# Kernel tuning notes

Hardware: AMD Instinct MI355X
Metric: run time of the kernel (lower is better)

Reference implementation:

```python
import jax, jax.numpy as jnp
import numpy as np

NUM_HEADS = 16


def setup_inputs() -> dict:
    key = jax.random.key(0)
    ks = jax.random.split(key, 7)
    B, N, D = 16, 512, 1024
    return {
        "x": jax.random.normal(ks[0], (B, N, D), dtype=jnp.float32),
        "spatial_encoding": jax.random.normal(ks[1], (B, N, N), dtype=jnp.float32),
        "edge_encoding": jax.random.normal(ks[2], (B, N, N), dtype=jnp.float32),
        "Wq": jax.random.normal(ks[3], (D, D), dtype=jnp.float32) * (D ** -0.5),
        "Wk": jax.random.normal(ks[4], (D, D), dtype=jnp.float32) * (D ** -0.5),
        "Wv": jax.random.normal(ks[5], (D, D), dtype=jnp.float32) * (D ** -0.5),
        "Wo": jax.random.normal(ks[6], (D, D), dtype=jnp.float32) * (D ** -0.5),
    }


def reference(x, spatial_encoding, edge_encoding, Wq, Wk, Wv, Wo):
    B, N, D = x.shape
    H = NUM_HEADS
    hd = D // H
    scale = D ** -0.5  # NOTE: source scales by hidden_dim**-0.5, not head_size**-0.5

    def split_heads(t):  # (B,N,D) -> (B,H,N,hd)
        return t.reshape(B, N, H, hd).transpose(0, 2, 1, 3)

    q = split_heads(x @ Wq.T)
    k = split_heads(x @ Wk.T)
    v = split_heads(x @ Wv.T)

    bias = (spatial_encoding + edge_encoding)[:, None]  # (B,1,N,N)
    a = jnp.einsum("bhnd,bhmd->bhnm", q, k) * scale + bias  # (B,H,N,N)

    # rows that are entirely zero (padded) are masked to -inf
    row_nonzero = jnp.any(a != 0, axis=-1, keepdims=True)  # (B,H,N,1)
    a = jnp.where(row_nonzero, a, -jnp.inf)
    p = jax.nn.softmax(a, axis=-1)
    p = jnp.where(jnp.isnan(p), 0.0, p)  # nan_to_num after softmax of all -inf rows

    o = jnp.einsum("bhnm,bhmd->bhnd", p, v)  # (B,H,N,hd)
    o = o.transpose(0, 2, 1, 3).reshape(B, N, D)
    return o @ Wo.T
```

## Files before the change

### kernel.cpp

```cpp
#include <hip/hip_runtime.h>
#include <cstdint>


typedef unsigned short u16;
typedef unsigned int   u32;
typedef __attribute__((ext_vector_type(8))) short bf8;
typedef __attribute__((ext_vector_type(4))) float f4;

__device__ __forceinline__ u16 f2bf(float x) {
  u32 u = __float_as_uint(x);
  u += 0x7FFF + ((u >> 16) & 1);
  return (u16)(u >> 16);
}

__device__ __forceinline__ float bf2f(u16 x) {
  return __uint_as_float(((u32)x) << 16);
}

__device__ __forceinline__ void gl2lds16(const void* g, void* l) {
  __builtin_amdgcn_global_load_lds(
      (const __attribute__((address_space(1))) u32*)g,
      (__attribute__((address_space(3))) u32*)l, 16, 0, 0);
}


__global__ __launch_bounds__(256) void cast_bf16(const float* __restrict__ src,
                                                 uint4* __restrict__ dst, int n8) {
  const int i = blockIdx.x * 256 + threadIdx.x;
  if (i >= n8) return;
  const float4* s = (const float4*)src;
  const float4 a = s[2 * i], c = s[2 * i + 1];
  uint4 o;
  o.x = (u32)f2bf(a.x) | ((u32)f2bf(a.y) << 16);
  o.y = (u32)f2bf(a.z) | ((u32)f2bf(a.w) << 16);
  o.z = (u32)f2bf(c.x) | ((u32)f2bf(c.y) << 16);
  o.w = (u32)f2bf(c.z) | ((u32)f2bf(c.w) << 16);
  dst[i] = o;
}

__global__ __launch_bounds__(256) void cast4_bf16(
    const float* __restrict__ s0, const float* __restrict__ s1,
    const float* __restrict__ s2, const float* __restrict__ s3,
    uint4* __restrict__ d0, uint4* __restrict__ d1,
    uint4* __restrict__ d2, uint4* __restrict__ d3) {
  const int i = blockIdx.x * 256 + threadIdx.x;
  const int w = i >> 17, j = i & 131071;
  const float* src = (w == 0) ? s0 : (w == 1) ? s1 : (w == 2) ? s2 : s3;
  uint4* dst = (w == 0) ? d0 : (w == 1) ? d1 : (w == 2) ? d2 : d3;
  const float4* s = (const float4*)src;
  const float4 a = s[2 * j], c = s[2 * j + 1];
  uint4 o;
  o.x = (u32)f2bf(a.x) | ((u32)f2bf(a.y) << 16);
  o.y = (u32)f2bf(a.z) | ((u32)f2bf(a.w) << 16);
  o.z = (u32)f2bf(c.x) | ((u32)f2bf(c.y) << 16);
  o.w = (u32)f2bf(c.z) | ((u32)f2bf(c.w) << 16);
  dst[j] = o;
}

__global__ __launch_bounds__(256) void bias_bf16(const float* __restrict__ s1,
                                                 const float* __restrict__ s2,
                                                 uint4* __restrict__ dst, int n8) {
  const int i = blockIdx.x * 256 + threadIdx.x;
  if (i >= n8) return;
  const float4* a4 = (const float4*)s1;
  const float4* b4 = (const float4*)s2;
  const float4 a = a4[2 * i], b = b4[2 * i];
  const float4 c = a4[2 * i + 1], d = b4[2 * i + 1];
  uint4 o;
  o.x = (u32)f2bf(a.x + b.x) | ((u32)f2bf(a.y + b.y) << 16);
  o.y = (u32)f2bf(a.z + b.z) | ((u32)f2bf(a.w + b.w) << 16);
  o.z = (u32)f2bf(c.x + d.x) | ((u32)f2bf(c.y + d.y) << 16);
  o.w = (u32)f2bf(c.z + d.z) | ((u32)f2bf(c.w + d.w) << 16);
  dst[i] = o;
}


__device__ __forceinline__ void gemm_core(const u16* __restrict__ A,
                                          const u16* __restrict__ Bt,
                                          int m0, int n0,
                                          u16* lA, u16* lB, f4 acc[4][4]) {
  const int tid  = threadIdx.x;
  const int wave = tid >> 6;
  const int lane = tid & 63;
  const int quad = lane >> 4;
  const int l16  = lane & 15;
  const int wm   = (wave >> 1) << 6;
  const int wn   = (wave & 1) << 6;
  const int srow = tid >> 3;
  const int scol = ((tid & 7) ^ (srow & 7)) << 3;
  const int c0   = (quad ^ (l16 & 7)) << 3;

  f4 zero = {0.f, 0.f, 0.f, 0.f};
#pragma unroll
  for (int mi = 0; mi < 4; mi++)
#pragma unroll
    for (int ni = 0; ni < 4; ni++) acc[mi][ni] = zero;

  const u16* Ab = A  + (size_t)(m0 + srow) * 1024 + scol;
  const u16* Bb = Bt + (size_t)(n0 + srow) * 1024 + scol;

  for (int k0 = 0; k0 < 1024; k0 += 64) {
    __syncthreads();
#pragma unroll
    for (int i = 0; i < 4; i++) {
      gl2lds16(Ab + (size_t)(i << 5) * 1024 + k0,
               (char*)lA + (((i << 8) + (wave << 6)) << 4));
      gl2lds16(Bb + (size_t)(i << 5) * 1024 + k0,
               (char*)lB + (((i << 8) + (wave << 6)) << 4));
    }
    __syncthreads();
#pragma unroll
    for (int kk = 0; kk < 64; kk += 32) {
      const int o = c0 ^ kk;
      bf8 af[4], bfr[4];
#pragma unroll
      for (int mi = 0; mi < 4; mi++)
        af[mi] = *(const bf8*)(lA + (wm + (mi << 4) + l16) * 64 + o);
#pragma unroll
      for (int ni = 0; ni < 4; ni++)
        bfr[ni] = *(const bf8*)(lB + (wn + (ni << 4) + l16) * 64 + o);
#pragma unroll
      for (int mi = 0; mi < 4; mi++)
#pragma unroll
        for (int ni = 0; ni < 4; ni++)
          acc[mi][ni] = __builtin_amdgcn_mfma_f32_16x16x32_bf16(
              af[mi], bfr[ni], acc[mi][ni], 0, 0, 0);
    }
  }
}


__global__ __launch_bounds__(256) void qkv_kernel(
    const u16* __restrict__ xb, const u16* __restrict__ wq,
    const u16* __restrict__ wk, const u16* __restrict__ wv,
    u16* __restrict__ Qh, u16* __restrict__ Kh, u16* __restrict__ Vt) {
  __shared__ __align__(16) u16 lA[128 * 64];
  __shared__ __align__(16) u16 lB[128 * 64];
  const int m0 = blockIdx.y << 7, n0 = blockIdx.x << 7;
  const int proj = blockIdx.z;
  const u16* W = (proj == 0) ? wq : (proj == 1) ? wk : wv;
  f4 acc[4][4];
  gemm_core(xb, W, m0, n0, lA, lB, acc);

  const int tid = threadIdx.x, wave = tid >> 6, lane = tid & 63;
  const int quad = lane >> 4, l16 = lane & 15;
  const int wm = (wave >> 1) << 6, wn = (wave & 1) << 6;

  if (proj == 2) {
#pragma unroll
    for (int mi = 0; mi < 4; mi++) {
      const int gmb = m0 + wm + (mi << 4) + (quad << 2);
      const int b = gmb >> 9, nb = gmb & 511;
#pragma unroll
      for (int ni = 0; ni < 4; ni++) {
        const int gn = n0 + wn + (ni << 4) + l16;
        const int h = gn >> 6, hdi = gn & 63;
        ushort4 pk;
        pk.x = f2bf(acc[mi][ni][0]);
        pk.y = f2bf(acc[mi][ni][1]);
        pk.z = f2bf(acc[mi][ni][2]);
        pk.w = f2bf(acc[mi][ni][3]);
        *(ushort4*)(Vt + ((size_t)((b << 4) + h) * 64 + hdi) * 512 + nb) = pk;
      }
    }
  } else {
    u16* dst = (proj == 0) ? Qh : Kh;
#pragma unroll
    for (int mi = 0; mi < 4; mi++) {
#pragma unroll
      for (int r = 0; r < 4; r++) {
        const int gm = m0 + wm + (mi << 4) + (quad << 2) + r;
        const int b = gm >> 9, n = gm & 511;
#pragma unroll
        for (int ni = 0; ni < 4; ni++) {
          const int gn = n0 + wn + (ni << 4) + l16;
          const int h = gn >> 6, hdi = gn & 63;
          dst[((size_t)((b << 4) + h) * 512 + n) * 64 + hdi] = f2bf(acc[mi][ni][r]);
        }
      }
    }
  }
}


__global__ __launch_bounds__(256) void oproj_kernel(const u16* __restrict__ Ob,
                                                    const u16* __restrict__ wo,
                                                    float* __restrict__ out) {
  __shared__ __align__(16) u16 lA[128 * 64];
  __shared__ __align__(16) u16 lB[128 * 64];
  const int m0 = blockIdx.y << 7, n0 = blockIdx.x << 7;
  f4 acc[4][4];
  gemm_core(Ob, wo, m0, n0, lA, lB, acc);

  const int tid = threadIdx.x, wave = tid >> 6, lane = tid & 63;
  const int quad = lane >> 4, l16 = lane & 15;
  const int wm = (wave >> 1) << 6, wn = (wave & 1) << 6;
#pragma unroll
  for (int mi = 0; mi < 4; mi++)
#pragma unroll
    for (int r = 0; r < 4; r++) {
      const int gm = m0 + wm + (mi << 4) + (quad << 2) + r;
#pragma unroll
      for (int ni = 0; ni < 4; ni++) {
        const int gn = n0 + wn + (ni << 4) + l16;
        out[(size_t)gm * 1024 + gn] = acc[mi][ni][r];
      }
    }
}


__global__ __launch_bounds__(256) void attn_kernel(
    const u16* __restrict__ Qh, const u16* __restrict__ Kh,
    const u16* __restrict__ Vt, const u16* __restrict__ Bb,
    u16* __restrict__ Ob) {
  __shared__ __align__(16) u16 sQ[64 * 64];
  __shared__ __align__(16) u16 sK[64 * 64];
  __shared__ __align__(16) u16 sV[64 * 64];
  __shared__ __align__(16) u16 sP[4 * 16 * 72];
  const int q0 = blockIdx.x << 6;
  const int h = blockIdx.y, b = blockIdx.z;
  const int tid = threadIdx.x, wave = tid >> 6, lane = tid & 63;
  const int quad = lane >> 4, l16 = lane & 15;
  const int c0  = (quad ^ (l16 & 7)) << 3;
  const int swb = (((tid & 7) ^ ((tid >> 3) & 7)) << 4);

  const u16* Qg = Qh + ((size_t)((b << 4) + h) * 512 + q0) * 64;
  const u16* Kg = Kh + (size_t)((b << 4) + h) * 512 * 64;
  const u16* Vg = Vt + (size_t)((b << 4) + h) * 64 * 512;
  const u16* Bg = Bb + (size_t)b * 512 * 512 + (size_t)q0 * 512;

#pragma unroll
  for (int i = 0; i < 2; i++) {
    const int e = (i << 8) + tid;
    gl2lds16((const char*)Qg + (e >> 3) * 128 + swb,
             (char*)sQ + (((i << 8) + (wave << 6)) << 4));
  }

  f4 o[4];
  f4 zero = {0.f, 0.f, 0.f, 0.f};
#pragma unroll
  for (int i = 0; i < 4; i++) o[i] = zero;
  float lsum[4] = {0.f, 0.f, 0.f, 0.f};
  const int qrl = (wave << 4) + (quad << 2);

  for (int j0 = 0; j0 < 512; j0 += 64) {
    __syncthreads();
#pragma unroll
    for (int i = 0; i < 2; i++) {
      const int e = (i << 8) + tid;
      gl2lds16((const char*)Kg + (size_t)j0 * 128 + (e >> 3) * 128 + swb,
               (char*)sK + (((i << 8) + (wave << 6)) << 4));
      gl2lds16((const char*)Vg + (size_t)(e >> 3) * 1024 + j0 * 2 + swb,
               (char*)sV + (((i << 8) + (wave << 6)) << 4));
    }
    __syncthreads();

    bf8 aq0 = *(const bf8*)(sQ + ((wave << 4) + l16) * 64 + c0);
    bf8 aq1 = *(const bf8*)(sQ + ((wave << 4) + l16) * 64 + (c0 ^ 32));
    u16* pw = sP + wave * (16 * 72);
#pragma unroll
    for (int nb = 0; nb < 4; nb++) {
      bf8 b0 = *(const bf8*)(sK + ((nb << 4) + l16) * 64 + c0);
      bf8 b1 = *(const bf8*)(sK + ((nb << 4) + l16) * 64 + (c0 ^ 32));
      f4 s = zero;
      s = __builtin_amdgcn_mfma_f32_16x16x32_bf16(aq0, b0, s, 0, 0, 0);
      s = __builtin_amdgcn_mfma_f32_16x16x32_bf16(aq1, b1, s, 0, 0, 0);
      const int gc = j0 + (nb << 4) + l16;
#pragma unroll
      for (int r = 0; r < 4; r++) {
        const float ev = __expf(s[r] * 0.03125f +
                                bf2f(Bg[(size_t)(qrl + r) * 512 + gc]));
        lsum[r] += ev;
        pw[((quad << 2) + r) * 72 + (nb << 4) + l16] = f2bf(ev);
      }
    }

    bf8 ap0 = *(const bf8*)(pw + l16 * 72 + (quad << 3));
    bf8 ap1 = *(const bf8*)(pw + l16 * 72 + 32 + (quad << 3));
#pragma unroll
    for (int db = 0; db < 4; db++) {
      bf8 v0 = *(const bf8*)(sV + ((db << 4) + l16) * 64 + c0);
      bf8 v1 = *(const bf8*)(sV + ((db << 4) + l16) * 64 + (c0 ^ 32));
      o[db] = __builtin_amdgcn_mfma_f32_16x16x32_bf16(ap0, v0, o[db], 0, 0, 0);
      o[db] = __builtin_amdgcn_mfma_f32_16x16x32_bf16(ap1, v1, o[db], 0, 0, 0);
    }
  }

#pragma unroll
  for (int r = 0; r < 4; r++) {
    float s = lsum[r];
    s += __shfl_xor(s, 1);
    s += __shfl_xor(s, 2);
    s += __shfl_xor(s, 4);
    s += __shfl_xor(s, 8);
    const float inv = 1.f / s;
    const int gr = q0 + qrl + r;
#pragma unroll
    for (int db = 0; db < 4; db++)
      Ob[(size_t)((b << 9) + gr) * 1024 + (h << 6) + (db << 4) + l16] =
          f2bf(o[db][r] * inv);
  }
}


extern "C" void kernel_launch(void* const* d_in, const int* in_sizes, int n_in,
                              void* d_out, int out_size, void* d_ws, size_t ws_size,
                              hipStream_t stream) {
  const float* x  = (const float*)d_in[0];
  const float* sp = (const float*)d_in[1];
  const float* ed = (const float*)d_in[2];
  const float* Wq = (const float*)d_in[3];
  const float* Wk = (const float*)d_in[4];
  const float* Wv = (const float*)d_in[5];
  const float* Wo = (const float*)d_in[6];
  float* out = (float*)d_out;

  char* w = (char*)d_ws;
  u16* xb  = (u16*)(w);
  u16* wqb = (u16*)(w + 16777216);
  u16* wkb = (u16*)(w + 18874368);
  u16* wvb = (u16*)(w + 20971520);
  u16* wob = (u16*)(w + 23068672);
  u16* Qh  = (u16*)(w + 25165824);
  u16* Kh  = (u16*)(w + 41943040);
  u16* Vt  = (u16*)(w + 58720256);
  u16* Ob  = (u16*)(w + 75497472);
  u16* Bb  = (u16*)(w + 92274688);

  cast_bf16<<<4096, 256, 0, stream>>>(x, (uint4*)xb, 1048576);
  cast4_bf16<<<2048, 256, 0, stream>>>(Wq, Wk, Wv, Wo,
                                       (uint4*)wqb, (uint4*)wkb,
                                       (uint4*)wvb, (uint4*)wob);
  bias_bf16<<<2048, 256, 0, stream>>>(sp, ed, (uint4*)Bb, 524288);

  qkv_kernel<<<dim3(8, 64, 3), 256, 0, stream>>>(xb, wqb, wkb, wvb, Qh, Kh, Vt);
  attn_kernel<<<dim3(8, 16, 16), 256, 0, stream>>>(Qh, Kh, Vt, Bb, Ob);
  oproj_kernel<<<dim3(8, 64, 1), 256, 0, stream>>>(Ob, wob, out);
}
```

Before: 278.9 us.

## Prepermute bias into MFMA fragment order and remap block order for L2 locality

The bias kernel now writes the summed spatial+edge bias in a tile layout matching each thread's MFMA accumulator fragment. The attention kernel can then fetch its 16 bias values per key tile with two 16-byte vector loads instead of 16 scattered 2-byte loads. The QKV, output-projection and attention grids also remap the flat block index so that blocks running at the same time share operand tiles (the same batch, or a group of M tiles) in cache. The bias prep kernel now does strided, uncoalesced reads of the fp32 inputs, and the swizzles add some index arithmetic.

```diff
diff --git a/kernel.cpp b/kernel.cpp
--- a/kernel.cpp
+++ b/kernel.cpp
@@ -57,21 +57,27 @@
   dst[j] = o;
 }
 
-__global__ __launch_bounds__(256) void bias_bf16(const float* __restrict__ s1,
-                                                 const float* __restrict__ s2,
-                                                 uint4* __restrict__ dst, int n8) {
-  const int i = blockIdx.x * 256 + threadIdx.x;
-  if (i >= n8) return;
-  const float4* a4 = (const float4*)s1;
-  const float4* b4 = (const float4*)s2;
-  const float4 a = a4[2 * i], b = b4[2 * i];
-  const float4 c = a4[2 * i + 1], d = b4[2 * i + 1];
-  uint4 o;
-  o.x = (u32)f2bf(a.x + b.x) | ((u32)f2bf(a.y + b.y) << 16);
-  o.y = (u32)f2bf(a.z + b.z) | ((u32)f2bf(a.w + b.w) << 16);
-  o.z = (u32)f2bf(c.x + d.x) | ((u32)f2bf(c.y + d.y) << 16);
-  o.w = (u32)f2bf(c.z + d.z) | ((u32)f2bf(c.w + d.w) << 16);
-  dst[i] = o;
+__global__ __launch_bounds__(256) void bias_perm(const float* __restrict__ sp,
+                                                 const float* __restrict__ ed,
+                                                 u16* __restrict__ Bp) {
+  const int jt = blockIdx.x, qt = blockIdx.y, b = blockIdx.z;
+  const int tid = threadIdx.x;
+  const int wave = tid >> 6, quad = (tid >> 4) & 3, l16 = tid & 15;
+  const int qrl = (wave << 4) + (quad << 2);
+  union { u16 a[16]; uint4 v[2]; } tmp;
+#pragma unroll
+  for (int nb = 0; nb < 4; nb++) {
+    const int col = (jt << 6) + (nb << 4) + l16;
+#pragma unroll
+    for (int r = 0; r < 4; r++) {
+      const int row = (qt << 6) + qrl + r;
+      const size_t idx = ((size_t)b << 18) + (size_t)row * 512 + col;
+      tmp.a[nb * 4 + r] = f2bf(sp[idx] + ed[idx]);
+    }
+  }
+  uint4* out = (uint4*)Bp + ((((size_t)b * 8 + qt) * 8 + jt) * 256 + tid) * 2;
+  out[0] = tmp.v[0];
+  out[1] = tmp.v[1];
 }
 
 
@@ -136,8 +142,11 @@
     u16* __restrict__ Qh, u16* __restrict__ Kh, u16* __restrict__ Vt) {
   __shared__ __align__(16) u16 lA[128 * 64];
   __shared__ __align__(16) u16 lB[128 * 64];
-  const int m0 = blockIdx.y << 7, n0 = blockIdx.x << 7;
-  const int proj = blockIdx.z;
+  const int flat = blockIdx.x + (blockIdx.y << 3) + (blockIdx.z << 9);
+  const int m_tile = (flat & 7) | (((flat >> 6) & 7) << 3);
+  const int n_tile = (flat >> 3) & 7;
+  const int proj = flat >> 9;
+  const int m0 = m_tile << 7, n0 = n_tile << 7;
   const u16* W = (proj == 0) ? wq : (proj == 1) ? wk : wv;
   f4 acc[4][4];
   gemm_core(xb, W, m0, n0, lA, lB, acc);
@@ -188,7 +197,9 @@
                                                     float* __restrict__ out) {
   __shared__ __align__(16) u16 lA[128 * 64];
   __shared__ __align__(16) u16 lB[128 * 64];
-  const int m0 = blockIdx.y << 7, n0 = blockIdx.x << 7;
+  const int flat = blockIdx.x + (blockIdx.y << 3);
+  const int m0 = ((flat & 7) | (((flat >> 6) & 7) << 3)) << 7;
+  const int n0 = ((flat >> 3) & 7) << 7;
   f4 acc[4][4];
   gemm_core(Ob, wo, m0, n0, lA, lB, acc);
 
@@ -211,14 +222,17 @@
 
 __global__ __launch_bounds__(256) void attn_kernel(
     const u16* __restrict__ Qh, const u16* __restrict__ Kh,
-    const u16* __restrict__ Vt, const u16* __restrict__ Bb,
+    const u16* __restrict__ Vt, const u16* __restrict__ Bp,
     u16* __restrict__ Ob) {
   __shared__ __align__(16) u16 sQ[64 * 64];
   __shared__ __align__(16) u16 sK[64 * 64];
   __shared__ __align__(16) u16 sV[64 * 64];
   __shared__ __align__(16) u16 sP[4 * 16 * 72];
-  const int q0 = blockIdx.x << 6;
-  const int h = blockIdx.y, b = blockIdx.z;
+  const int flat = blockIdx.x + (blockIdx.y << 3) + (blockIdx.z << 7);
+  const int qt = (flat >> 3) & 7;
+  const int h  = (flat >> 6) & 15;
+  const int b  = (flat & 7) | (((flat >> 10) & 1) << 3);
+  const int q0 = qt << 6;
   const int tid = threadIdx.x, wave = tid >> 6, lane = tid & 63;
   const int quad = lane >> 4, l16 = lane & 15;
   const int c0  = (quad ^ (l16 & 7)) << 3;
@@ -227,7 +241,7 @@
   const u16* Qg = Qh + ((size_t)((b << 4) + h) * 512 + q0) * 64;
   const u16* Kg = Kh + (size_t)((b << 4) + h) * 512 * 64;
   const u16* Vg = Vt + (size_t)((b << 4) + h) * 64 * 512;
-  const u16* Bg = Bb + (size_t)b * 512 * 512 + (size_t)q0 * 512;
+  const uint4* Bpg = (const uint4*)Bp + (((size_t)b * 8 + qt) * 8 * 256 + tid) * 2;
 
 #pragma unroll
   for (int i = 0; i < 2; i++) {
@@ -244,6 +258,10 @@
   const int qrl = (wave << 4) + (quad << 2);
 
   for (int j0 = 0; j0 < 512; j0 += 64) {
+    const uint4 bc0 = Bpg[(j0 >> 6) * 512];
+    const uint4 bc1 = Bpg[(j0 >> 6) * 512 + 1];
+    const u32 bw[8] = {bc0.x, bc0.y, bc0.z, bc0.w, bc1.x, bc1.y, bc1.z, bc1.w};
+
     __syncthreads();
 #pragma unroll
     for (int i = 0; i < 2; i++) {
@@ -265,11 +283,11 @@
       f4 s = zero;
       s = __builtin_amdgcn_mfma_f32_16x16x32_bf16(aq0, b0, s, 0, 0, 0);
       s = __builtin_amdgcn_mfma_f32_16x16x32_bf16(aq1, b1, s, 0, 0, 0);
-      const int gc = j0 + (nb << 4) + l16;
 #pragma unroll
       for (int r = 0; r < 4; r++) {
-        const float ev = __expf(s[r] * 0.03125f +
-                                bf2f(Bg[(size_t)(qrl + r) * 512 + gc]));
+        const u32 w = bw[nb * 2 + (r >> 1)];
+        const float bias = bf2f((r & 1) ? (u16)(w >> 16) : (u16)(w & 0xFFFF));
+        const float ev = __expf(s[r] * 0.03125f + bias);
         lsum[r] += ev;
         pw[((quad << 2) + r) * 72 + (nb << 4) + l16] = f2bf(ev);
       }
@@ -325,15 +343,15 @@
   u16* Kh  = (u16*)(w + 41943040);
   u16* Vt  = (u16*)(w + 58720256);
   u16* Ob  = (u16*)(w + 75497472);
-  u16* Bb  = (u16*)(w + 92274688);
+  u16* Bp  = (u16*)(w + 92274688);
 
   cast_bf16<<<4096, 256, 0, stream>>>(x, (uint4*)xb, 1048576);
   cast4_bf16<<<2048, 256, 0, stream>>>(Wq, Wk, Wv, Wo,
                                        (uint4*)wqb, (uint4*)wkb,
                                        (uint4*)wvb, (uint4*)wob);
-  bias_bf16<<<2048, 256, 0, stream>>>(sp, ed, (uint4*)Bb, 524288);
+  bias_perm<<<dim3(8, 8, 16), 256, 0, stream>>>(sp, ed, Bp);
 
   qkv_kernel<<<dim3(8, 64, 3), 256, 0, stream>>>(xb, wqb, wkb, wvb, Qh, Kh, Vt);
-  attn_kernel<<<dim3(8, 16, 16), 256, 0, stream>>>(Qh, Kh, Vt, Bb, Ob);
+  attn_kernel<<<dim3(8, 16, 16), 256, 0, stream>>>(Qh, Kh, Vt, Bp, Ob);
   oproj_kernel<<<dim3(8, 64, 1), 256, 0, stream>>>(Ob, wob, out);
 }
```

After: 251.7 us. 1.11x faster.
